# Kernel optimization log

Hardware: AMD Instinct MI355X
Metric: run time of the kernel (lower is better)

Reference implementation:

```python
import jax, jax.numpy as jnp
import numpy as np

N_NODES = 20000
N_EDGES = 320000
N_FEAT = 128
MLP_HID = 64
N_GRAPHS = 16
N_LAYERS = 5
EPS = 1e-5


def setup_inputs() -> dict:
    key = jax.random.key(0)
    ks = jax.random.split(key, 8)
    x = jax.random.normal(ks[0], (N_NODES, N_FEAT), dtype=jnp.float32)
    edge_index = jax.random.randint(ks[1], (2, N_EDGES), 0, N_NODES, dtype=jnp.int64)
    batch = jnp.sort(jax.random.randint(ks[2], (N_NODES,), 0, N_GRAPHS, dtype=jnp.int64))
    W1 = jax.random.normal(ks[3], (N_LAYERS, N_FEAT, MLP_HID), dtype=jnp.float32) * 0.05
    b1 = jnp.zeros((N_LAYERS, MLP_HID), dtype=jnp.float32)
    W2 = jax.random.normal(ks[4], (N_LAYERS, MLP_HID, N_FEAT), dtype=jnp.float32) * 0.05
    b2 = jnp.zeros((N_LAYERS, N_FEAT), dtype=jnp.float32)
    gn_weight = jnp.ones((N_LAYERS, N_FEAT), dtype=jnp.float32)
    gn_bias = jnp.zeros((N_LAYERS, N_FEAT), dtype=jnp.float32)
    gn_scale = jnp.ones((N_LAYERS, N_FEAT), dtype=jnp.float32)
    lin_w = jax.random.normal(ks[5], (N_FEAT, 1), dtype=jnp.float32) * 0.05
    lin_b = jnp.zeros((1,), dtype=jnp.float32)
    return {"x": x, "edge_index": edge_index, "batch": batch,
            "W1": W1, "b1": b1, "W2": W2, "b2": b2,
            "gn_weight": gn_weight, "gn_bias": gn_bias, "gn_scale": gn_scale,
            "lin_w": lin_w, "lin_b": lin_b}


def _conv(h, src, dst, W1, b1, W2, b2):
    # message MLP is per-source-node, so compute MLP(x) once per node,
    # then gather by src and scatter-add to dst. Self loops add m[i] at i.
    m = jax.nn.relu(h @ W1 + b1) @ W2 + b2  # [N, C]
    return jax.ops.segment_sum(m[src], dst, num_segments=N_NODES) + m


def _graph_norm(h, batch, cnt, w, b, a):
    mean = jax.ops.segment_sum(h, batch, num_segments=N_GRAPHS) / cnt  # [G, C]
    out = h - a * mean[batch]
    var = jax.ops.segment_sum(out * out, batch, num_segments=N_GRAPHS) / cnt
    out = out * jax.lax.rsqrt(var[batch] + EPS)
    return w * out + b


def reference(x, edge_index, batch, W1, b1, W2, b2, gn_weight, gn_bias, gn_scale, lin_w, lin_b):
    src, dst = edge_index[0], edge_index[1]
    cnt = jax.ops.segment_sum(jnp.ones((N_NODES, 1), x.dtype), batch,
                              num_segments=N_GRAPHS)
    cnt = jnp.maximum(cnt, 1.0)  # [G, 1]
    h = x
    for i in range(N_LAYERS):
        g = _conv(h, src, dst, W1[i], b1[i], W2[i], b2[i])
        g = _graph_norm(g, batch, cnt, gn_weight[i], gn_bias[i], gn_scale[i])
        g = jax.nn.relu(g)  # dropout is identity in eval mode
        h = g if i == 0 else g + h  # residual from layer 2 onward
    pooled = jax.ops.segment_sum(h, batch, num_segments=N_GRAPHS) / cnt  # [G, C]
    return pooled @ lin_w + lin_b  # [G, 1]
```

## Files before the change

kernel.cpp:

```cpp
#include <hip/hip_runtime.h>

#define N_NODES 20000
#define N_EDGES 320000
#define N_FEAT 128
#define MLP_HID 64
#define N_GRAPHS 16
#define N_LAYERS 5
#define EPS 1e-5f

typedef __attribute__((ext_vector_type(8))) short short8;
typedef __attribute__((ext_vector_type(4))) float f32x4;

__device__ inline float bf2f(unsigned short u) { return __uint_as_float(((unsigned)u) << 16); }
__device__ inline unsigned short f2bf(float f) {
  unsigned u = __float_as_uint(f);
  u += 0x7FFF + ((u >> 16) & 1);
  return (unsigned short)(u >> 16);
}


__global__ __launch_bounds__(256) void k_deg(const int* __restrict__ dst, int* __restrict__ deg) {
  int e = blockIdx.x * 256 + threadIdx.x;
  atomicAdd(&deg[dst[e]], 1);
}

__global__ __launch_bounds__(1024) void k_scan(const int* __restrict__ deg, int* __restrict__ rowptr,
                                               int* __restrict__ cursor, const int* __restrict__ batch,
                                               float* __restrict__ cntf, float* __restrict__ pooled) {
  __shared__ int sdata[1024];
  __shared__ int spos[17];
  constexpr int CH = 20;
  int t = threadIdx.x;
  for (int i = t; i < N_GRAPHS * N_FEAT; i += 1024) pooled[i] = 0.0f;
  int base = t * CH;
  int loc[CH];
  int partial = 0;
#pragma unroll
  for (int i = 0; i < CH; i++) {
    int idx = base + i;
    int v = (idx < N_NODES) ? deg[idx] : 0;
    loc[i] = v;
    partial += v;
  }
  sdata[t] = partial;
  __syncthreads();
  for (int off = 1; off < 1024; off <<= 1) {
    int v = (t >= off) ? sdata[t - off] : 0;
    __syncthreads();
    sdata[t] += v;
    __syncthreads();
  }
  int run = sdata[t] - partial;
#pragma unroll
  for (int i = 0; i < CH; i++) {
    int idx = base + i;
    if (idx < N_NODES) {
      rowptr[idx] = run;
      cursor[idx] = run;
      run += loc[i];
    }
  }
  if (t == 1023) rowptr[N_NODES] = sdata[1023];
  if (t < 17) {
    int lo = 0, hi = N_NODES;
    while (lo < hi) {
      int mid = (lo + hi) >> 1;
      if (batch[mid] < t) lo = mid + 1; else hi = mid;
    }
    spos[t] = lo;
  }
  __syncthreads();
  if (t < N_GRAPHS) cntf[t] = fmaxf((float)(spos[t + 1] - spos[t]), 1.0f);
}

__global__ __launch_bounds__(256) void k_fill(const int* __restrict__ src, const int* __restrict__ dst,
                                              int* __restrict__ cursor, int* __restrict__ src_sorted) {
  int e = blockIdx.x * 256 + threadIdx.x;
  int d = dst[e];
  int p = atomicAdd(&cursor[d], 1);
  src_sorted[p] = src[e];
}


__global__ __launch_bounds__(256) void k_prep(const float* __restrict__ W1, const float* __restrict__ W2,
                                              unsigned short* __restrict__ w1t, unsigned short* __restrict__ w2t) {
  int idx = blockIdx.x * 256 + threadIdx.x;
  if (idx < 40960) {
    int l = idx >> 13, rem = idx & 8191;
    int n = rem >> 7, k = rem & 127;
    w1t[idx] = f2bf(W1[l * 8192 + k * 64 + n]);
  } else {
    int j = idx - 40960;
    int l = j >> 13, rem = j & 8191;
    int n = rem >> 6, k = rem & 63;
    w2t[j] = f2bf(W2[l * 8192 + k * 128 + n]);
  }
}


#define PADK 136
#define PADH 72

__global__ __launch_bounds__(256) void k_mlp(const float* __restrict__ hin, unsigned short* __restrict__ mout,
                                             const unsigned short* __restrict__ w1t,
                                             const unsigned short* __restrict__ w2t,
                                             const float* __restrict__ b1, const float* __restrict__ b2) {
  __shared__ __align__(16) short hS[64 * PADK];
  __shared__ __align__(16) short w1S[64 * PADK];
  __shared__ __align__(16) short hidS[64 * PADH];
  __shared__ __align__(16) short w2S[128 * PADH];
  __shared__ float b1S[64];
  __shared__ float b2S[128];
  int t = threadIdx.x;
  int r0 = blockIdx.x * 64;
#pragma unroll
  for (int i = 0; i < 8; i++) {
    int idx = t + i * 256;
    int row = idx >> 5, c4 = idx & 31;
    float4 v = (r0 + row < N_NODES) ? ((const float4*)hin)[(size_t)(r0 + row) * 32 + c4]
                                    : make_float4(0.f, 0.f, 0.f, 0.f);
    ushort4 s;
    s.x = f2bf(v.x); s.y = f2bf(v.y); s.z = f2bf(v.z); s.w = f2bf(v.w);
    *(ushort4*)&hS[row * PADK + c4 * 4] = s;
  }
#pragma unroll
  for (int i = 0; i < 4; i++) {
    int idx = t + i * 256;
    *(int4*)&w1S[(idx >> 4) * PADK + (idx & 15) * 8] = ((const int4*)w1t)[idx];
    *(int4*)&w2S[(idx >> 3) * PADH + (idx & 7) * 8] = ((const int4*)w2t)[idx];
  }
  if (t < 64) b1S[t] = b1[t];
  else if (t < 192) b2S[t - 64] = b2[t - 64];
  __syncthreads();

  int w = t >> 6, lane = t & 63, lm = lane & 15, quad = lane >> 4;
  int mrow = w * 16 + lm;
  int orow = w * 16 + quad * 4;

  f32x4 zero = {0.f, 0.f, 0.f, 0.f};
  f32x4 acc[4] = {zero, zero, zero, zero};
#pragma unroll
  for (int k0 = 0; k0 < 128; k0 += 32) {
    short8 a = *(const short8*)&hS[mrow * PADK + k0 + quad * 8];
#pragma unroll
    for (int nt = 0; nt < 4; nt++) {
      short8 b = *(const short8*)&w1S[(nt * 16 + lm) * PADK + k0 + quad * 8];
      acc[nt] = __builtin_amdgcn_mfma_f32_16x16x32_bf16(a, b, acc[nt], 0, 0, 0);
    }
  }
#pragma unroll
  for (int nt = 0; nt < 4; nt++) {
    int col = nt * 16 + lm;
    float bb = b1S[col];
#pragma unroll
    for (int r = 0; r < 4; r++)
      hidS[(orow + r) * PADH + col] = (short)f2bf(fmaxf(acc[nt][r] + bb, 0.0f));
  }
  __syncthreads();

  f32x4 acc2[8] = {zero, zero, zero, zero, zero, zero, zero, zero};
#pragma unroll
  for (int k0 = 0; k0 < 64; k0 += 32) {
    short8 a = *(const short8*)&hidS[mrow * PADH + k0 + quad * 8];
#pragma unroll
    for (int nt = 0; nt < 8; nt++) {
      short8 b = *(const short8*)&w2S[(nt * 16 + lm) * PADH + k0 + quad * 8];
      acc2[nt] = __builtin_amdgcn_mfma_f32_16x16x32_bf16(a, b, acc2[nt], 0, 0, 0);
    }
  }
#pragma unroll
  for (int nt = 0; nt < 8; nt++) {
    int col = nt * 16 + lm;
    float bb = b2S[col];
#pragma unroll
    for (int r = 0; r < 4; r++)
      hS[(orow + r) * PADK + col] = (short)f2bf(acc2[nt][r] + bb);
  }
  __syncthreads();
#pragma unroll
  for (int i = 0; i < 4; i++) {
    int idx = t + i * 256;
    int row = idx >> 4, cc = idx & 15;
    if (r0 + row < N_NODES)
      ((int4*)mout)[(size_t)(r0 + row) * 16 + cc] = *(const int4*)&hS[row * PADK + cc * 8];
  }
}


__global__ __launch_bounds__(256) void k_scatter(const unsigned short* __restrict__ mbf, float* __restrict__ g,
                                                 const int* __restrict__ rowptr, const int* __restrict__ srcs,
                                                 float* __restrict__ s1, float* __restrict__ s2) {
  if (blockIdx.x == 0) {
    for (int i = threadIdx.x; i < N_GRAPHS * N_FEAT; i += 256) { s1[i] = 0.0f; s2[i] = 0.0f; }
  }
  int node = (blockIdx.x * 256 + threadIdx.x) >> 6;
  int lane = threadIdx.x & 63;
  int quarter = lane >> 4;
  int q16 = lane & 15;
  const float4* m4 = (const float4*)mbf;
  float acc[8];
  union BU { float4 f; unsigned short u[8]; };
  if (quarter == 0) {
    BU U; U.f = m4[(size_t)node * 16 + q16];
#pragma unroll
    for (int j = 0; j < 8; j++) acc[j] = bf2f(U.u[j]);
  } else {
#pragma unroll
    for (int j = 0; j < 8; j++) acc[j] = 0.0f;
  }
  int e = rowptr[node], e1 = rowptr[node + 1];
  for (; e + 16 <= e1; e += 16) {
    int i0 = srcs[e + quarter];
    int i1 = srcs[e + 4 + quarter];
    int i2 = srcs[e + 8 + quarter];
    int i3 = srcs[e + 12 + quarter];
    BU U0, U1, U2, U3;
    U0.f = m4[(size_t)i0 * 16 + q16];
    U1.f = m4[(size_t)i1 * 16 + q16];
    U2.f = m4[(size_t)i2 * 16 + q16];
    U3.f = m4[(size_t)i3 * 16 + q16];
#pragma unroll
    for (int j = 0; j < 8; j++)
      acc[j] += (bf2f(U0.u[j]) + bf2f(U1.u[j])) + (bf2f(U2.u[j]) + bf2f(U3.u[j]));
  }
  for (; e + 4 <= e1; e += 4) {
    BU U0; U0.f = m4[(size_t)srcs[e + quarter] * 16 + q16];
#pragma unroll
    for (int j = 0; j < 8; j++) acc[j] += bf2f(U0.u[j]);
  }
  if (e + quarter < e1) {
    BU U0; U0.f = m4[(size_t)srcs[e + quarter] * 16 + q16];
#pragma unroll
    for (int j = 0; j < 8; j++) acc[j] += bf2f(U0.u[j]);
  }
#pragma unroll
  for (int j = 0; j < 8; j++) {
    acc[j] += __shfl_xor(acc[j], 16);
    acc[j] += __shfl_xor(acc[j], 32);
  }
  if (quarter == 0) {
    float4* g4 = (float4*)(g + (size_t)node * 128 + q16 * 8);
    g4[0] = make_float4(acc[0], acc[1], acc[2], acc[3]);
    g4[1] = make_float4(acc[4], acc[5], acc[6], acc[7]);
  }
}


#define STAT_CHUNK 8

__global__ __launch_bounds__(128) void k_stats(const float* __restrict__ in, const int* __restrict__ batch,
                                               float* __restrict__ s1, float* __restrict__ s2) {
  int n0 = blockIdx.x * STAT_CHUNK;
  int c = threadIdx.x;
  int curg = batch[n0];
  float a1 = 0.0f, a2 = 0.0f;
#pragma unroll
  for (int k = 0; k < STAT_CHUNK; k++) {
    int n = n0 + k;
    int gg = batch[n];
    if (gg != curg) {
      atomicAdd(&s1[curg * 128 + c], a1);
      atomicAdd(&s2[curg * 128 + c], a2);
      a1 = 0.0f; a2 = 0.0f;
      curg = gg;
    }
    float v = in[(size_t)n * 128 + c];
    a1 += v;
    a2 += v * v;
  }
  atomicAdd(&s1[curg * 128 + c], a1);
  atomicAdd(&s2[curg * 128 + c], a2);
}

__global__ __launch_bounds__(128) void k_segsum(const float* __restrict__ in, const int* __restrict__ batch,
                                                float* __restrict__ outbuf) {
  int n0 = blockIdx.x * STAT_CHUNK;
  int c = threadIdx.x;
  int curg = batch[n0];
  float acc = 0.0f;
#pragma unroll
  for (int k = 0; k < STAT_CHUNK; k++) {
    int n = n0 + k;
    int gg = batch[n];
    if (gg != curg) {
      atomicAdd(&outbuf[curg * 128 + c], acc);
      acc = 0.0f;
      curg = gg;
    }
    acc += in[(size_t)n * 128 + c];
  }
  atomicAdd(&outbuf[curg * 128 + c], acc);
}


__global__ __launch_bounds__(256) void k_apply(const float* __restrict__ gin, float* __restrict__ h,
                                               const int* __restrict__ batch,
                                               const float* __restrict__ s1, const float* __restrict__ s2,
                                               const float* __restrict__ cntf,
                                               const float* __restrict__ w, const float* __restrict__ b,
                                               const float* __restrict__ a, int residual) {
  int idx = blockIdx.x * 256 + threadIdx.x;
  int n = idx >> 5, c4 = idx & 31;
  int gg = batch[n];
  float invc = 1.0f / cntf[gg];
  float4 sm = ((const float4*)s1)[gg * 32 + c4];
  float4 se = ((const float4*)s2)[gg * 32 + c4];
  float4 av = ((const float4*)a)[c4];
  float4 wv = ((const float4*)w)[c4];
  float4 bv = ((const float4*)b)[c4];
  float4 gv = ((const float4*)gin)[idx];
  float4 hv = make_float4(0.f, 0.f, 0.f, 0.f);
  if (residual) hv = ((const float4*)h)[idx];
  float4 o;
#define APPLY1(X)                                                          \
  {                                                                        \
    float mean = sm.X * invc;                                              \
    float ex2 = se.X * invc;                                               \
    float ac = av.X;                                                       \
    float var = fmaxf(ex2 - mean * mean * (2.0f * ac - ac * ac), 0.0f);    \
    float d = gv.X - ac * mean;                                            \
    float y = wv.X * (d * rsqrtf(var + EPS)) + bv.X;                       \
    y = fmaxf(y, 0.0f);                                                    \
    o.X = residual ? (y + hv.X) : y;                                       \
  }
  APPLY1(x) APPLY1(y) APPLY1(z) APPLY1(w)
#undef APPLY1
  ((float4*)h)[idx] = o;
}


__global__ __launch_bounds__(256) void k_final(const float* __restrict__ pooled, const float* __restrict__ cntf,
                                               const float* __restrict__ lw, const float* __restrict__ lb,
                                               float* __restrict__ out) {
  int lane = threadIdx.x & 63, wave = threadIdx.x >> 6;
  for (int gi = 0; gi < 4; gi++) {
    int gidx = wave * 4 + gi;
    float s = pooled[gidx * 128 + lane] * lw[lane] + pooled[gidx * 128 + 64 + lane] * lw[64 + lane];
    for (int o = 32; o >= 1; o >>= 1) s += __shfl_down(s, o);
    if (lane == 0) out[gidx] = s / cntf[gidx] + lb[0];
  }
}


extern "C" void kernel_launch(void* const* d_in, const int* in_sizes, int n_in,
                              void* d_out, int out_size, void* d_ws, size_t ws_size,
                              hipStream_t stream) {
  const float* x = (const float*)d_in[0];
  const int* ei = (const int*)d_in[1];
  const int* batch = (const int*)d_in[2];
  const float* W1 = (const float*)d_in[3];
  const float* b1 = (const float*)d_in[4];
  const float* W2 = (const float*)d_in[5];
  const float* b2 = (const float*)d_in[6];
  const float* gnw = (const float*)d_in[7];
  const float* gnb = (const float*)d_in[8];
  const float* gna = (const float*)d_in[9];
  const float* lw = (const float*)d_in[10];
  const float* lb = (const float*)d_in[11];
  float* out = (float*)d_out;

  const int* srcI = ei;
  const int* dstI = ei + N_EDGES;

  char* p = (char*)d_ws;
  float* hbuf = (float*)(p + 0);
  unsigned short* mbuf = (unsigned short*)(p + 10240000);
  float* gbuf = (float*)(p + 20480000);
  int* src_sorted = (int*)(p + 30720000);
  int* rowptr = (int*)(p + 32000000);
  int* cursor = (int*)(p + 32080128);
  int* deg = (int*)(p + 32160256);
  float* cntf = (float*)(p + 32240512);
  float* s1buf = (float*)(p + 32240640);
  float* s2buf = (float*)(p + 32248832);
  float* pooled = (float*)(p + 32257024);
  unsigned short* w1t = (unsigned short*)(p + 32265216);
  unsigned short* w2t = (unsigned short*)(p + 32347136);

  hipMemsetAsync(deg, 0, N_NODES * sizeof(int), stream);
  k_deg<<<N_EDGES / 256, 256, 0, stream>>>(dstI, deg);
  k_scan<<<1, 1024, 0, stream>>>(deg, rowptr, cursor, batch, cntf, pooled);
  k_fill<<<N_EDGES / 256, 256, 0, stream>>>(srcI, dstI, cursor, src_sorted);
  k_prep<<<320, 256, 0, stream>>>(W1, W2, w1t, w2t);

  const float* hin = x;
  for (int i = 0; i < N_LAYERS; i++) {
    k_mlp<<<(N_NODES + 63) / 64, 256, 0, stream>>>(hin, mbuf, w1t + (size_t)i * 8192, w2t + (size_t)i * 8192,
                                                   b1 + (size_t)i * 64, b2 + (size_t)i * 128);
    k_scatter<<<N_NODES / 4, 256, 0, stream>>>(mbuf, gbuf, rowptr, src_sorted, s1buf, s2buf);
    k_stats<<<N_NODES / STAT_CHUNK, 128, 0, stream>>>(gbuf, batch, s1buf, s2buf);
    k_apply<<<N_NODES * N_FEAT / 4 / 256, 256, 0, stream>>>(gbuf, hbuf, batch, s1buf, s2buf, cntf,
                                                            gnw + (size_t)i * 128, gnb + (size_t)i * 128,
                                                            gna + (size_t)i * 128, i > 0 ? 1 : 0);
    hin = hbuf;
  }

  k_segsum<<<N_NODES / STAT_CHUNK, 128, 0, stream>>>(hbuf, batch, pooled);
  k_final<<<1, 256, 0, stream>>>(pooled, cntf, lw, lb, out);
}
```

Measured before the change: 334.6 us.

## Fuse graph-norm stats into scatter and apply into next-layer MLP

Per-graph sum and sum-of-squares statistics are now reduced in shared memory inside the scatter kernel, which removes the separate stats kernel and its extra full read of g. The normalize/ReLU/residual apply step is fused into the next layer's MLP kernel, so h is turned into bf16 in registers and fed straight to the MFMA GEMMs without a separate pass. The last layer's apply is fused with mean pooling, and the memset is folded into k_prep, with per-layer stat buffers zeroed once up front. This cuts the launch count and global traffic, in exchange for a heavier MLP kernel that must also do elementwise apply work.

```diff
diff --git a/kernel.cpp b/kernel.cpp
--- a/kernel.cpp
+++ b/kernel.cpp
@@ -18,6 +18,17 @@
   return (unsigned short)(u >> 16);
 }
 
+__device__ __forceinline__ float apply1(float gvx, float hvx, float smx, float sex,
+                                        float invc, float ac, float wx, float bx) {
+  float mean = smx * invc;
+  float ex2 = sex * invc;
+  float var = fmaxf(ex2 - mean * mean * (2.0f * ac - ac * ac), 0.0f);
+  float d = gvx - ac * mean;
+  float y = wx * (d * rsqrtf(var + EPS)) + bx;
+  y = fmaxf(y, 0.0f);
+  return y + hvx;
+}
+
 
 __global__ __launch_bounds__(256) void k_deg(const int* __restrict__ dst, int* __restrict__ deg) {
   int e = blockIdx.x * 256 + threadIdx.x;
@@ -26,12 +37,14 @@
 
 __global__ __launch_bounds__(1024) void k_scan(const int* __restrict__ deg, int* __restrict__ rowptr,
                                                int* __restrict__ cursor, const int* __restrict__ batch,
-                                               float* __restrict__ cntf, float* __restrict__ pooled) {
+                                               float* __restrict__ cntf, float* __restrict__ pooled,
+                                               float* __restrict__ s1, float* __restrict__ s2) {
   __shared__ int sdata[1024];
   __shared__ int spos[17];
   constexpr int CH = 20;
   int t = threadIdx.x;
   for (int i = t; i < N_GRAPHS * N_FEAT; i += 1024) pooled[i] = 0.0f;
+  for (int i = t; i < N_LAYERS * N_GRAPHS * N_FEAT; i += 1024) { s1[i] = 0.0f; s2[i] = 0.0f; }
   int base = t * CH;
   int loc[CH];
   int partial = 0;
@@ -83,8 +96,10 @@
 
 
 __global__ __launch_bounds__(256) void k_prep(const float* __restrict__ W1, const float* __restrict__ W2,
-                                              unsigned short* __restrict__ w1t, unsigned short* __restrict__ w2t) {
+                                              unsigned short* __restrict__ w1t, unsigned short* __restrict__ w2t,
+                                              int* __restrict__ deg) {
   int idx = blockIdx.x * 256 + threadIdx.x;
+  if (idx < N_NODES) deg[idx] = 0;
   if (idx < 40960) {
     int l = idx >> 13, rem = idx & 8191;
     int n = rem >> 7, k = rem & 127;
@@ -100,6 +115,64 @@
 
 #define PADK 136
 #define PADH 72
+
+__device__ __forceinline__ void mlp_body(int t, int r0,
+                                         short* hS, short* w1S, short* hidS, short* w2S,
+                                         const float* b1S, const float* b2S,
+                                         unsigned short* __restrict__ mout) {
+  int w = t >> 6, lane = t & 63, lm = lane & 15, quad = lane >> 4;
+  int mrow = w * 16 + lm;
+  int orow = w * 16 + quad * 4;
+
+  f32x4 zero = {0.f, 0.f, 0.f, 0.f};
+  f32x4 acc[4] = {zero, zero, zero, zero};
+#pragma unroll
+  for (int k0 = 0; k0 < 128; k0 += 32) {
+    short8 a = *(const short8*)&hS[mrow * PADK + k0 + quad * 8];
+#pragma unroll
+    for (int nt = 0; nt < 4; nt++) {
+      short8 b = *(const short8*)&w1S[(nt * 16 + lm) * PADK + k0 + quad * 8];
+      acc[nt] = __builtin_amdgcn_mfma_f32_16x16x32_bf16(a, b, acc[nt], 0, 0, 0);
+    }
+  }
+#pragma unroll
+  for (int nt = 0; nt < 4; nt++) {
+    int col = nt * 16 + lm;
+    float bb = b1S[col];
+#pragma unroll
+    for (int r = 0; r < 4; r++)
+      hidS[(orow + r) * PADH + col] = (short)f2bf(fmaxf(acc[nt][r] + bb, 0.0f));
+  }
+  __syncthreads();
+
+  f32x4 acc2[8] = {zero, zero, zero, zero, zero, zero, zero, zero};
+#pragma unroll
+  for (int k0 = 0; k0 < 64; k0 += 32) {
+    short8 a = *(const short8*)&hidS[mrow * PADH + k0 + quad * 8];
+#pragma unroll
+    for (int nt = 0; nt < 8; nt++) {
+      short8 b = *(const short8*)&w2S[(nt * 16 + lm) * PADH + k0 + quad * 8];
+      acc2[nt] = __builtin_amdgcn_mfma_f32_16x16x32_bf16(a, b, acc2[nt], 0, 0, 0);
+    }
+  }
+#pragma unroll
+  for (int nt = 0; nt < 8; nt++) {
+    int col = nt * 16 + lm;
+    float bb = b2S[col];
+#pragma unroll
+    for (int r = 0; r < 4; r++)
+      hS[(orow + r) * PADK + col] = (short)f2bf(acc2[nt][r] + bb);
+  }
+  __syncthreads();
+#pragma unroll
+  for (int i = 0; i < 4; i++) {
+    int idx = t + i * 256;
+    int row = idx >> 4, cc = idx & 15;
+    if (r0 + row < N_NODES)
+      ((int4*)mout)[(size_t)(r0 + row) * 16 + cc] = *(const int4*)&hS[row * PADK + cc * 8];
+  }
+}
+
 
 __global__ __launch_bounds__(256) void k_mlp(const float* __restrict__ hin, unsigned short* __restrict__ mout,
                                              const unsigned short* __restrict__ w1t,
@@ -132,69 +205,79 @@
   if (t < 64) b1S[t] = b1[t];
   else if (t < 192) b2S[t - 64] = b2[t - 64];
   __syncthreads();
-
-  int w = t >> 6, lane = t & 63, lm = lane & 15, quad = lane >> 4;
-  int mrow = w * 16 + lm;
-  int orow = w * 16 + quad * 4;
-
-  f32x4 zero = {0.f, 0.f, 0.f, 0.f};
-  f32x4 acc[4] = {zero, zero, zero, zero};
-#pragma unroll
-  for (int k0 = 0; k0 < 128; k0 += 32) {
-    short8 a = *(const short8*)&hS[mrow * PADK + k0 + quad * 8];
-#pragma unroll
-    for (int nt = 0; nt < 4; nt++) {
-      short8 b = *(const short8*)&w1S[(nt * 16 + lm) * PADK + k0 + quad * 8];
-      acc[nt] = __builtin_amdgcn_mfma_f32_16x16x32_bf16(a, b, acc[nt], 0, 0, 0);
-    }
-  }
-#pragma unroll
-  for (int nt = 0; nt < 4; nt++) {
-    int col = nt * 16 + lm;
-    float bb = b1S[col];
-#pragma unroll
-    for (int r = 0; r < 4; r++)
-      hidS[(orow + r) * PADH + col] = (short)f2bf(fmaxf(acc[nt][r] + bb, 0.0f));
-  }
-  __syncthreads();
-
-  f32x4 acc2[8] = {zero, zero, zero, zero, zero, zero, zero, zero};
-#pragma unroll
-  for (int k0 = 0; k0 < 64; k0 += 32) {
-    short8 a = *(const short8*)&hidS[mrow * PADH + k0 + quad * 8];
-#pragma unroll
-    for (int nt = 0; nt < 8; nt++) {
-      short8 b = *(const short8*)&w2S[(nt * 16 + lm) * PADH + k0 + quad * 8];
-      acc2[nt] = __builtin_amdgcn_mfma_f32_16x16x32_bf16(a, b, acc2[nt], 0, 0, 0);
-    }
-  }
-#pragma unroll
-  for (int nt = 0; nt < 8; nt++) {
-    int col = nt * 16 + lm;
-    float bb = b2S[col];
-#pragma unroll
-    for (int r = 0; r < 4; r++)
-      hS[(orow + r) * PADK + col] = (short)f2bf(acc2[nt][r] + bb);
-  }
-  __syncthreads();
+  mlp_body(t, r0, hS, w1S, hidS, w2S, b1S, b2S, mout);
+}
+
+
+__global__ __launch_bounds__(256) void k_apply_mlp(const float* __restrict__ gin, float* __restrict__ h,
+                                                   const int* __restrict__ batch,
+                                                   const float* __restrict__ s1, const float* __restrict__ s2,
+                                                   const float* __restrict__ cntf,
+                                                   const float* __restrict__ gw, const float* __restrict__ gb,
+                                                   const float* __restrict__ ga, int residual,
+                                                   unsigned short* __restrict__ mout,
+                                                   const unsigned short* __restrict__ w1t,
+                                                   const unsigned short* __restrict__ w2t,
+                                                   const float* __restrict__ b1, const float* __restrict__ b2) {
+  __shared__ __align__(16) short hS[64 * PADK];
+  __shared__ __align__(16) short w1S[64 * PADK];
+  __shared__ __align__(16) short hidS[64 * PADH];
+  __shared__ __align__(16) short w2S[128 * PADH];
+  __shared__ float b1S[64];
+  __shared__ float b2S[128];
+  int t = threadIdx.x;
+  int r0 = blockIdx.x * 64;
 #pragma unroll
   for (int i = 0; i < 4; i++) {
     int idx = t + i * 256;
-    int row = idx >> 4, cc = idx & 15;
-    if (r0 + row < N_NODES)
-      ((int4*)mout)[(size_t)(r0 + row) * 16 + cc] = *(const int4*)&hS[row * PADK + cc * 8];
-  }
+    *(int4*)&w1S[(idx >> 4) * PADK + (idx & 15) * 8] = ((const int4*)w1t)[idx];
+    *(int4*)&w2S[(idx >> 3) * PADH + (idx & 7) * 8] = ((const int4*)w2t)[idx];
+  }
+  if (t < 64) b1S[t] = b1[t];
+  else if (t < 192) b2S[t - 64] = b2[t - 64];
+  int c4 = t & 31;
+  float4 av = ((const float4*)ga)[c4];
+  float4 wv = ((const float4*)gw)[c4];
+  float4 bv = ((const float4*)gb)[c4];
+#pragma unroll
+  for (int i = 0; i < 8; i++) {
+    int row = (t >> 5) + i * 8;
+    int n = r0 + row;
+    ushort4 s;
+    s.x = 0; s.y = 0; s.z = 0; s.w = 0;
+    if (n < N_NODES) {
+      int gg = batch[n];
+      float invc = 1.0f / cntf[gg];
+      float4 sm = ((const float4*)s1)[gg * 32 + c4];
+      float4 se = ((const float4*)s2)[gg * 32 + c4];
+      float4 gv = ((const float4*)gin)[(size_t)n * 32 + c4];
+      float4 hv = make_float4(0.f, 0.f, 0.f, 0.f);
+      if (residual) hv = ((const float4*)h)[(size_t)n * 32 + c4];
+      float4 o;
+      o.x = apply1(gv.x, hv.x, sm.x, se.x, invc, av.x, wv.x, bv.x);
+      o.y = apply1(gv.y, hv.y, sm.y, se.y, invc, av.y, wv.y, bv.y);
+      o.z = apply1(gv.z, hv.z, sm.z, se.z, invc, av.z, wv.z, bv.z);
+      o.w = apply1(gv.w, hv.w, sm.w, se.w, invc, av.w, wv.w, bv.w);
+      ((float4*)h)[(size_t)n * 32 + c4] = o;
+      s.x = f2bf(o.x); s.y = f2bf(o.y); s.z = f2bf(o.z); s.w = f2bf(o.w);
+    }
+    *(ushort4*)&hS[row * PADK + c4 * 4] = s;
+  }
+  __syncthreads();
+  mlp_body(t, r0, hS, w1S, hidS, w2S, b1S, b2S, mout);
 }
 
 
 __global__ __launch_bounds__(256) void k_scatter(const unsigned short* __restrict__ mbf, float* __restrict__ g,
                                                  const int* __restrict__ rowptr, const int* __restrict__ srcs,
+                                                 const int* __restrict__ batch,
                                                  float* __restrict__ s1, float* __restrict__ s2) {
-  if (blockIdx.x == 0) {
-    for (int i = threadIdx.x; i < N_GRAPHS * N_FEAT; i += 256) { s1[i] = 0.0f; s2[i] = 0.0f; }
-  }
-  int node = (blockIdx.x * 256 + threadIdx.x) >> 6;
-  int lane = threadIdx.x & 63;
+  __shared__ float sS1[4][128];
+  __shared__ float sS2[4][128];
+  int t = threadIdx.x;
+  int node = (blockIdx.x * 256 + t) >> 6;
+  int w = t >> 6;
+  int lane = t & 63;
   int quarter = lane >> 4;
   int q16 = lane & 15;
   const float4* m4 = (const float4*)mbf;
@@ -242,90 +325,75 @@
     float4* g4 = (float4*)(g + (size_t)node * 128 + q16 * 8);
     g4[0] = make_float4(acc[0], acc[1], acc[2], acc[3]);
     g4[1] = make_float4(acc[4], acc[5], acc[6], acc[7]);
-  }
-}
-
-
-#define STAT_CHUNK 8
-
-__global__ __launch_bounds__(128) void k_stats(const float* __restrict__ in, const int* __restrict__ batch,
-                                               float* __restrict__ s1, float* __restrict__ s2) {
-  int n0 = blockIdx.x * STAT_CHUNK;
-  int c = threadIdx.x;
-  int curg = batch[n0];
-  float a1 = 0.0f, a2 = 0.0f;
-#pragma unroll
-  for (int k = 0; k < STAT_CHUNK; k++) {
-    int n = n0 + k;
-    int gg = batch[n];
-    if (gg != curg) {
-      atomicAdd(&s1[curg * 128 + c], a1);
-      atomicAdd(&s2[curg * 128 + c], a2);
-      a1 = 0.0f; a2 = 0.0f;
-      curg = gg;
-    }
-    float v = in[(size_t)n * 128 + c];
-    a1 += v;
-    a2 += v * v;
-  }
-  atomicAdd(&s1[curg * 128 + c], a1);
-  atomicAdd(&s2[curg * 128 + c], a2);
-}
-
-__global__ __launch_bounds__(128) void k_segsum(const float* __restrict__ in, const int* __restrict__ batch,
-                                                float* __restrict__ outbuf) {
-  int n0 = blockIdx.x * STAT_CHUNK;
-  int c = threadIdx.x;
-  int curg = batch[n0];
-  float acc = 0.0f;
-#pragma unroll
-  for (int k = 0; k < STAT_CHUNK; k++) {
-    int n = n0 + k;
-    int gg = batch[n];
-    if (gg != curg) {
-      atomicAdd(&outbuf[curg * 128 + c], acc);
-      acc = 0.0f;
-      curg = gg;
-    }
-    acc += in[(size_t)n * 128 + c];
-  }
-  atomicAdd(&outbuf[curg * 128 + c], acc);
-}
-
-
-__global__ __launch_bounds__(256) void k_apply(const float* __restrict__ gin, float* __restrict__ h,
-                                               const int* __restrict__ batch,
-                                               const float* __restrict__ s1, const float* __restrict__ s2,
-                                               const float* __restrict__ cntf,
-                                               const float* __restrict__ w, const float* __restrict__ b,
-                                               const float* __restrict__ a, int residual) {
-  int idx = blockIdx.x * 256 + threadIdx.x;
+#pragma unroll
+    for (int j = 0; j < 8; j++) {
+      float v = acc[j];
+      sS1[w][q16 * 8 + j] = v;
+      sS2[w][q16 * 8 + j] = v * v;
+    }
+  }
+  __syncthreads();
+  int n0 = blockIdx.x * 4;
+  int gA = batch[n0], gB = batch[n0 + 3];
+  if (t < 128) {
+    if (gA == gB) {
+      atomicAdd(&s1[gA * 128 + t], sS1[0][t] + sS1[1][t] + sS1[2][t] + sS1[3][t]);
+    } else {
+#pragma unroll
+      for (int ww = 0; ww < 4; ww++) atomicAdd(&s1[batch[n0 + ww] * 128 + t], sS1[ww][t]);
+    }
+  } else {
+    int c = t - 128;
+    if (gA == gB) {
+      atomicAdd(&s2[gA * 128 + c], sS2[0][c] + sS2[1][c] + sS2[2][c] + sS2[3][c]);
+    } else {
+#pragma unroll
+      for (int ww = 0; ww < 4; ww++) atomicAdd(&s2[batch[n0 + ww] * 128 + c], sS2[ww][c]);
+    }
+  }
+}
+
+
+__global__ __launch_bounds__(256) void k_apply_pool(const float* __restrict__ gin, const float* __restrict__ h,
+                                                    const int* __restrict__ batch,
+                                                    const float* __restrict__ s1, const float* __restrict__ s2,
+                                                    const float* __restrict__ cntf,
+                                                    const float* __restrict__ gw, const float* __restrict__ gb,
+                                                    const float* __restrict__ ga,
+                                                    float* __restrict__ pooled) {
+  __shared__ float pS[8][128];
+  int t = threadIdx.x;
+  int idx = blockIdx.x * 256 + t;
   int n = idx >> 5, c4 = idx & 31;
   int gg = batch[n];
   float invc = 1.0f / cntf[gg];
   float4 sm = ((const float4*)s1)[gg * 32 + c4];
   float4 se = ((const float4*)s2)[gg * 32 + c4];
-  float4 av = ((const float4*)a)[c4];
-  float4 wv = ((const float4*)w)[c4];
-  float4 bv = ((const float4*)b)[c4];
+  float4 av = ((const float4*)ga)[c4];
+  float4 wv = ((const float4*)gw)[c4];
+  float4 bv = ((const float4*)gb)[c4];
   float4 gv = ((const float4*)gin)[idx];
-  float4 hv = make_float4(0.f, 0.f, 0.f, 0.f);
-  if (residual) hv = ((const float4*)h)[idx];
+  float4 hv = ((const float4*)h)[idx];
   float4 o;
-#define APPLY1(X)                                                          \
-  {                                                                        \
-    float mean = sm.X * invc;                                              \
-    float ex2 = se.X * invc;                                               \
-    float ac = av.X;                                                       \
-    float var = fmaxf(ex2 - mean * mean * (2.0f * ac - ac * ac), 0.0f);    \
-    float d = gv.X - ac * mean;                                            \
-    float y = wv.X * (d * rsqrtf(var + EPS)) + bv.X;                       \
-    y = fmaxf(y, 0.0f);                                                    \
-    o.X = residual ? (y + hv.X) : y;                                       \
-  }
-  APPLY1(x) APPLY1(y) APPLY1(z) APPLY1(w)
-#undef APPLY1
-  ((float4*)h)[idx] = o;
+  o.x = apply1(gv.x, hv.x, sm.x, se.x, invc, av.x, wv.x, bv.x);
+  o.y = apply1(gv.y, hv.y, sm.y, se.y, invc, av.y, wv.y, bv.y);
+  o.z = apply1(gv.z, hv.z, sm.z, se.z, invc, av.z, wv.z, bv.z);
+  o.w = apply1(gv.w, hv.w, sm.w, se.w, invc, av.w, wv.w, bv.w);
+  *(float4*)&pS[t >> 5][c4 * 4] = o;
+  __syncthreads();
+  int n0 = blockIdx.x * 8;
+  int gA = batch[n0], gB = batch[n0 + 7];
+  if (t < 128) {
+    if (gA == gB) {
+      float s = 0.f;
+#pragma unroll
+      for (int ww = 0; ww < 8; ww++) s += pS[ww][t];
+      atomicAdd(&pooled[gA * 128 + t], s);
+    } else {
+#pragma unroll
+      for (int ww = 0; ww < 8; ww++) atomicAdd(&pooled[batch[n0 + ww] * 128 + t], pS[ww][t]);
+    }
+  }
 }
 
 
@@ -365,36 +433,41 @@
   char* p = (char*)d_ws;
   float* hbuf = (float*)(p + 0);
   unsigned short* mbuf = (unsigned short*)(p + 10240000);
-  float* gbuf = (float*)(p + 20480000);
-  int* src_sorted = (int*)(p + 30720000);
-  int* rowptr = (int*)(p + 32000000);
-  int* cursor = (int*)(p + 32080128);
-  int* deg = (int*)(p + 32160256);
-  float* cntf = (float*)(p + 32240512);
-  float* s1buf = (float*)(p + 32240640);
-  float* s2buf = (float*)(p + 32248832);
-  float* pooled = (float*)(p + 32257024);
-  unsigned short* w1t = (unsigned short*)(p + 32265216);
-  unsigned short* w2t = (unsigned short*)(p + 32347136);
-
-  hipMemsetAsync(deg, 0, N_NODES * sizeof(int), stream);
+  float* gbuf = (float*)(p + 15360000);
+  int* src_sorted = (int*)(p + 25600000);
+  int* rowptr = (int*)(p + 26880000);
+  int* cursor = (int*)(p + 26960128);
+  int* deg = (int*)(p + 27040128);
+  float* cntf = (float*)(p + 27120128);
+  float* s1buf = (float*)(p + 27120192);
+  float* s2buf = (float*)(p + 27161152);
+  float* pooled = (float*)(p + 27202112);
+  unsigned short* w1t = (unsigned short*)(p + 27210304);
+  unsigned short* w2t = (unsigned short*)(p + 27292224);
+
+  k_prep<<<320, 256, 0, stream>>>(W1, W2, w1t, w2t, deg);
   k_deg<<<N_EDGES / 256, 256, 0, stream>>>(dstI, deg);
-  k_scan<<<1, 1024, 0, stream>>>(deg, rowptr, cursor, batch, cntf, pooled);
+  k_scan<<<1, 1024, 0, stream>>>(deg, rowptr, cursor, batch, cntf, pooled, s1buf, s2buf);
   k_fill<<<N_EDGES / 256, 256, 0, stream>>>(srcI, dstI, cursor, src_sorted);
-  k_prep<<<320, 256, 0, stream>>>(W1, W2, w1t, w2t);
-
-  const float* hin = x;
+
+  k_mlp<<<(N_NODES + 63) / 64, 256, 0, stream>>>(x, mbuf, w1t, w2t, b1, b2);
+
   for (int i = 0; i < N_LAYERS; i++) {
-    k_mlp<<<(N_NODES + 63) / 64, 256, 0, stream>>>(hin, mbuf, w1t + (size_t)i * 8192, w2t + (size_t)i * 8192,
-                                                   b1 + (size_t)i * 64, b2 + (size_t)i * 128);
-    k_scatter<<<N_NODES / 4, 256, 0, stream>>>(mbuf, gbuf, rowptr, src_sorted, s1buf, s2buf);
-    k_stats<<<N_NODES / STAT_CHUNK, 128, 0, stream>>>(gbuf, batch, s1buf, s2buf);
-    k_apply<<<N_NODES * N_FEAT / 4 / 256, 256, 0, stream>>>(gbuf, hbuf, batch, s1buf, s2buf, cntf,
-                                                            gnw + (size_t)i * 128, gnb + (size_t)i * 128,
-                                                            gna + (size_t)i * 128, i > 0 ? 1 : 0);
-    hin = hbuf;
-  }
-
-  k_segsum<<<N_NODES / STAT_CHUNK, 128, 0, stream>>>(hbuf, batch, pooled);
+    k_scatter<<<N_NODES / 4, 256, 0, stream>>>(mbuf, gbuf, rowptr, src_sorted, batch,
+                                               s1buf + (size_t)i * 2048, s2buf + (size_t)i * 2048);
+    if (i < N_LAYERS - 1) {
+      int li = i + 1;
+      k_apply_mlp<<<(N_NODES + 63) / 64, 256, 0, stream>>>(
+          gbuf, hbuf, batch, s1buf + (size_t)i * 2048, s2buf + (size_t)i * 2048, cntf,
+          gnw + (size_t)i * 128, gnb + (size_t)i * 128, gna + (size_t)i * 128, i > 0 ? 1 : 0,
+          mbuf, w1t + (size_t)li * 8192, w2t + (size_t)li * 8192,
+          b1 + (size_t)li * 64, b2 + (size_t)li * 128);
+    } else {
+      k_apply_pool<<<N_NODES / 8, 256, 0, stream>>>(
+          gbuf, hbuf, batch, s1buf + (size_t)i * 2048, s2buf + (size_t)i * 2048, cntf,
+          gnw + (size_t)i * 128, gnb + (size_t)i * 128, gna + (size_t)i * 128, pooled);
+    }
+  }
+
   k_final<<<1, 256, 0, stream>>>(pooled, cntf, lw, lb, out);
 }
```

Result: slower. 396.4 us (+18.5%).
